# Optimization experiments

Hardware: AMD Instinct MI355X
Metric: run time of the kernel (lower is better)

Reference implementation:

```python
import jax, jax.numpy as jnp
import numpy as np

D_MODEL = 1024
NUM_HEADS = 16
D_HEAD = D_MODEL // NUM_HEADS
B, S = 2, 2048


def setup_inputs() -> dict:
    key = jax.random.key(0)
    ks = jax.random.split(key, 12)
    s = 0.02
    return {
        "query": jax.random.normal(ks[0], (B, S, D_MODEL), jnp.float32),
        "key": jax.random.normal(ks[1], (B, S, D_MODEL), jnp.float32),
        "value": jax.random.normal(ks[2], (B, S, D_MODEL), jnp.float32),
        "mask": jnp.ones((B, 1, 1, S), jnp.float32),
        "W_q": jax.random.normal(ks[3], (D_MODEL, D_MODEL), jnp.float32) * s,
        "b_q": jnp.zeros((D_MODEL,), jnp.float32),
        "W_k": jax.random.normal(ks[4], (D_MODEL, D_MODEL), jnp.float32) * s,
        "b_k": jnp.zeros((D_MODEL,), jnp.float32),
        "W_v": jax.random.normal(ks[5], (D_MODEL, D_MODEL), jnp.float32) * s,
        "b_v": jnp.zeros((D_MODEL,), jnp.float32),
        "W_o": jax.random.normal(ks[6], (D_MODEL, D_MODEL), jnp.float32) * s,
        "b_o": jnp.zeros((D_MODEL,), jnp.float32),
    }


def reference(query, key, value, mask, W_q, b_q, W_k, b_k, W_v, b_v, W_o, b_o):
    # Linear projections (torch nn.Linear: x @ W.T + b; here W stored as [in, out])
    q = query @ W_q + b_q
    k = key @ W_k + b_k
    v = value @ W_v + b_v
    # [B, S, D] -> [B, H, S, Dh]
    def split_heads(x):
        b, s, _ = x.shape
        return x.reshape(b, s, NUM_HEADS, D_HEAD).transpose(0, 2, 1, 3)
    q, k, v = split_heads(q), split_heads(k), split_heads(v)
    # scaled dot-product attention; full [B,H,Sq,Sk] matrix (faithful to source)
    logits = jnp.einsum("bhqd,bhkd->bhqk", q, k) / jnp.sqrt(jnp.float32(D_HEAD))
    logits = logits + (1.0 - mask) * (-1e9)
    attn = jax.nn.softmax(logits, axis=-1)
    # dropout is identity in eval mode
    ctx = jnp.einsum("bhqk,bhkd->bhqd", attn, v)
    ctx = ctx.transpose(0, 2, 1, 3).reshape(ctx.shape[0], -1, D_MODEL)
    out = ctx @ W_o + b_o
    return out, attn
```

## Files before the change

### kernel.cpp

```cpp
#include <hip/hip_runtime.h>
#include <hip/hip_bf16.h>

#define BATCH 2
#define SEQ 2048
#define DM 1024
#define NH 16
#define DH 64
#define MTOT (BATCH*SEQ)

typedef __attribute__((ext_vector_type(8))) short bf16x8;
typedef __attribute__((ext_vector_type(4))) float f32x4;
typedef __attribute__((ext_vector_type(16))) float f32x16;
typedef __attribute__((ext_vector_type(4))) float float4v;
typedef __attribute__((ext_vector_type(8))) unsigned short u16x8;
typedef __attribute__((ext_vector_type(4))) unsigned short u16x4;

#define GLDS16(g, l) __builtin_amdgcn_global_load_lds(                         \
    (const __attribute__((address_space(1))) void*)(g),                        \
    (__attribute__((address_space(3))) void*)(l), 16, 0, 0)

static __device__ __forceinline__ float bf2f(unsigned short u) {
    unsigned int x = ((unsigned int)u) << 16;
    float f; __builtin_memcpy(&f, &x, 4); return f;
}
static __device__ __forceinline__ unsigned short f2bf(float f) {
    unsigned int x; __builtin_memcpy(&x, &f, 4);
    x += 0x7fffu + ((x >> 16) & 1);
    return (unsigned short)(x >> 16);
}
static __device__ __forceinline__ unsigned int cvt_pk_bf16(float a, float b) {
    unsigned int r;
    asm volatile("v_cvt_pk_bf16_f32 %0, %1, %2" : "=v"(r) : "v"(a), "v"(b));
    return r;
}

__global__ __launch_bounds__(256) void prep_kernel(
    const float* __restrict__ q, const float* __restrict__ k, const float* __restrict__ v,
    unsigned short* __restrict__ oq, unsigned short* __restrict__ ok_, unsigned short* __restrict__ ov,
    const float* __restrict__ w0, const float* __restrict__ w1,
    const float* __restrict__ w2, const float* __restrict__ w3,
    unsigned short* __restrict__ t0, unsigned short* __restrict__ t1,
    unsigned short* __restrict__ t2, unsigned short* __restrict__ t3) {
    __shared__ float tile[64][65];
    const int bx = blockIdx.x, t = threadIdx.x;
    if (bx < 6144) {
        const int slab = bx >> 11, bxr = bx & 2047;
        const float* in = slab == 0 ? q : (slab == 1 ? k : v);
        unsigned short* out = slab == 0 ? oq : (slab == 1 ? ok_ : ov);
        size_t i = ((size_t)bxr * 256 + t) * 8;
        float4v a = *(const float4v*)(in + i);
        float4v b = *(const float4v*)(in + i + 4);
        u16x8 r;
        r[0]=f2bf(a[0]); r[1]=f2bf(a[1]); r[2]=f2bf(a[2]); r[3]=f2bf(a[3]);
        r[4]=f2bf(b[0]); r[5]=f2bf(b[1]); r[6]=f2bf(b[2]); r[7]=f2bf(b[3]);
        *(u16x8*)(out + i) = r;
    } else {
        const int i2 = bx - 6144;
        const int z = i2 >> 8, rem = i2 & 255;
        const float* w = z==0 ? w0 : z==1 ? w1 : z==2 ? w2 : w3;
        unsigned short* wt = z==0 ? t0 : z==1 ? t1 : z==2 ? t2 : t3;
        const int k0 = (rem & 15) * 64, n0 = (rem >> 4) * 64;
        const int tr = t >> 4, tc = t & 15;
#pragma unroll
        for (int i = 0; i < 4; ++i) {
            float4v val = *(const float4v*)(w + (size_t)(k0 + tr + 16*i) * DM + n0 + tc*4);
            tile[tr + 16*i][tc*4 + 0] = val[0];
            tile[tr + 16*i][tc*4 + 1] = val[1];
            tile[tr + 16*i][tc*4 + 2] = val[2];
            tile[tr + 16*i][tc*4 + 3] = val[3];
        }
        __syncthreads();
#pragma unroll
        for (int i = 0; i < 4; ++i) {
            u16x4 o;
#pragma unroll
            for (int j = 0; j < 4; ++j) o[j] = f2bf(tile[tc*4 + j][tr + 16*i]);
            *(u16x4*)(wt + (size_t)(n0 + tr + 16*i) * DM + k0 + tc*4) = o;
        }
    }
}

template<int OUTMODE>
static __device__ __forceinline__ void gemm_body(
    const unsigned short* __restrict__ A, const unsigned short* __restrict__ Bt,
    const float* __restrict__ bias, void* __restrict__ Cout,
    unsigned short* a_lds, unsigned short* b_lds) {
    constexpr int BM = 128, BN = 64, BK = 64, NT = DM / BK;
    const int tid = threadIdx.x;
    const int m0 = blockIdx.y * BM, n0 = blockIdx.x * BN;
    const int w = tid >> 6, l = tid & 63;
    const int lr = l & 15, lg = l >> 4;
    const int wm = (w >> 1) * 64, wn = (w & 1) * 32;
    f32x4 acc[4][2] = {};

    auto stage = [&](int buf, int kt) {
        const int k0 = kt * BK;
#pragma unroll
        for (int i = 0; i < 4; ++i) {
            int u = i*256 + tid;
            int row = u >> 3, slot = u & 7;
            int sc = (slot ^ (row & 7)) * 8;
            GLDS16(A + (size_t)(m0 + row)*DM + k0 + sc, a_lds + buf*BM*BK + u*8);
        }
#pragma unroll
        for (int i = 0; i < 2; ++i) {
            int u = i*256 + tid;
            int row = u >> 3, slot = u & 7;
            int sc = (slot ^ (row & 7)) * 8;
            GLDS16(Bt + (size_t)(n0 + row)*DM + k0 + sc, b_lds + buf*BN*BK + u*8);
        }
    };

    stage(0, 0);
    for (int kt = 0; kt < NT; ++kt) {
        __syncthreads();
        if (kt < NT-1) stage((kt+1)&1, kt+1);
        const char* ab = (const char*)(a_lds + (kt&1)*BM*BK);
        const char* bb = (const char*)(b_lds + (kt&1)*BN*BK);
        bf16x8 af[4][2], bfr[2][2];
#pragma unroll
        for (int r = 0; r < 4; ++r)
#pragma unroll
            for (int kc = 0; kc < 2; ++kc) {
                int row = wm + r*16 + lr;
                af[r][kc] = *(const bf16x8*)(ab + row*128 + ((kc*64 + lg*16) ^ ((row&7)<<4)));
            }
#pragma unroll
        for (int c = 0; c < 2; ++c)
#pragma unroll
            for (int kc = 0; kc < 2; ++kc) {
                int row = wn + c*16 + lr;
                bfr[c][kc] = *(const bf16x8*)(bb + row*128 + ((kc*64 + lg*16) ^ ((row&7)<<4)));
            }
#pragma unroll
        for (int r = 0; r < 4; ++r)
#pragma unroll
            for (int c = 0; c < 2; ++c)
#pragma unroll
                for (int kc = 0; kc < 2; ++kc)
                    acc[r][c] = __builtin_amdgcn_mfma_f32_16x16x32_bf16(af[r][kc], bfr[c][kc], acc[r][c], 0, 0, 0);
    }

#pragma unroll
    for (int r = 0; r < 4; ++r)
#pragma unroll
        for (int c = 0; c < 2; ++c) {
            int m = m0 + wm + r*16 + lg*4;
            int n = n0 + wn + c*16 + lr;
            float bb = bias[n];
            if constexpr (OUTMODE == 1) {
                float* o = (float*)Cout;
#pragma unroll
                for (int j = 0; j < 4; ++j) o[(size_t)(m+j)*DM + n] = acc[r][c][j] + bb;
            } else if constexpr (OUTMODE == 0) {
                unsigned short* o = (unsigned short*)Cout;
#pragma unroll
                for (int j = 0; j < 4; ++j) o[(size_t)(m+j)*DM + n] = f2bf(acc[r][c][j] + bb);
            } else {
                unsigned short* o = (unsigned short*)Cout;
                int bb_ = m >> 11, kk = m & (SEQ-1);
                int bh = bb_ * NH + (n >> 6), d = n & 63;
                u16x4 ov;
#pragma unroll
                for (int j = 0; j < 4; ++j) ov[j] = f2bf(acc[r][c][j] + bb);
                *(u16x4*)(o + ((size_t)bh*DH + d)*SEQ + kk) = ov;
            }
        }
}

__global__ __launch_bounds__(256, 3) void gemm_qkv_kernel(
    const unsigned short* __restrict__ A0, const unsigned short* __restrict__ A1, const unsigned short* __restrict__ A2,
    const unsigned short* __restrict__ B0, const unsigned short* __restrict__ B1, const unsigned short* __restrict__ B2,
    const float* __restrict__ c0, const float* __restrict__ c1, const float* __restrict__ c2,
    unsigned short* __restrict__ O0, unsigned short* __restrict__ O1, unsigned short* __restrict__ O2) {
    __shared__ __align__(16) unsigned short smem[2*128*64 + 2*64*64];
    const int z = blockIdx.z;
    const unsigned short* A = z==0 ? A0 : z==1 ? A1 : A2;
    const unsigned short* B = z==0 ? B0 : z==1 ? B1 : B2;
    const float* c = z==0 ? c0 : z==1 ? c1 : c2;
    unsigned short* O = z==0 ? O0 : z==1 ? O1 : O2;
    if (z == 2) gemm_body<2>(A, B, c, O, smem, smem + 2*128*64);
    else        gemm_body<0>(A, B, c, O, smem, smem + 2*128*64);
}

__global__ __launch_bounds__(256, 3) void gemm_out_kernel(
    const unsigned short* __restrict__ A, const unsigned short* __restrict__ Bt,
    const float* __restrict__ bias, float* __restrict__ Cout) {
    __shared__ __align__(16) unsigned short smem[2*128*64 + 2*64*64];
    gemm_body<1>(A, Bt, bias, Cout, smem, smem + 2*128*64);
}

__global__ __launch_bounds__(512, 4) void attn_kernel(
    const unsigned short* __restrict__ qw, const unsigned short* __restrict__ kw,
    const unsigned short* __restrict__ vtg, const float* __restrict__ mask,
    float* __restrict__ attn_out, unsigned short* __restrict__ ctx) {
    constexpr int QB = 128, KB = 64, NT2 = SEQ / KB / 2;
    __shared__ __align__(16) unsigned short smem[4*KB*DH + 4*KB*DH + 4096];
    unsigned short* kbuf = smem;
    unsigned short* vbuf = smem + 4*KB*DH;
    float* madd_f = (float*)(smem + 8*KB*DH);
    const int tid = threadIdx.x, w = tid >> 6, l = tid & 63;
    const int hh = w >> 2, ws = w & 3;
    const int q32 = l & 31, hi = l >> 5;
    const int u0 = (blockIdx.x & 7) * 64 + (blockIdx.x >> 3);
    const int qblk = u0 & 15, bh = u0 >> 4;
    const int b = bh >> 4, h = bh & 15;
    const int q0 = qblk * QB;
    const int q = q0 + ws*32 + q32;
    const int kbase = hh * (SEQ/2);

    {
        int idx = tid * 4;
        float4v m4 = *(const float4v*)(mask + (size_t)b*SEQ + idx);
        float4v md;
#pragma unroll
        for (int r = 0; r < 4; ++r) md[r] = (1.0f - m4[r]) * (-1e9f);
        *(float4v*)(madd_f + idx) = md;
    }

    bf16x8 qf[4];
    {
        const unsigned short* qp = qw + ((size_t)(b*SEQ + q))*DM + h*DH + hi*8;
#pragma unroll
        for (int ks = 0; ks < 4; ++ks) {
            bf16x8 t = *(const bf16x8*)(qp + ks*16);
#pragma unroll
            for (int j = 0; j < 8; ++j) t[j] = (short)f2bf(bf2f((unsigned short)t[j]) * 0.125f);
            qf[ks] = t;
        }
    }

    auto stageK = [&](int buf, int kt) {
#pragma unroll
        for (int hf = 0; hf < 2; ++hf) {
            int row = tid >> 3, slot = tid & 7;
            int sc = (slot ^ (row & 7)) * 8;
            const unsigned short* base = kw + ((size_t)(b*SEQ + hf*(SEQ/2) + kt*KB + row))*DM + h*DH;
            GLDS16(base + sc, kbuf + (buf*2 + hf)*KB*DH + tid*8);
        }
    };
    auto stageV = [&](int buf, int kt) {
#pragma unroll
        for (int hf = 0; hf < 2; ++hf) {
            int row = tid >> 3, slot = tid & 7;
            int sc = (slot ^ (row & 7)) * 8;
            const unsigned short* base = vtg + ((size_t)bh*DH + row)*SEQ + hf*(SEQ/2) + kt*KB;
            GLDS16(base + sc, vbuf + (buf*2 + hf)*KB*DH + tid*8);
        }
    };

    float rs = 0.f;
    stageK(0, 0);
    for (int kt = 0; kt < NT2; ++kt) {
        __syncthreads();
        if (kt < NT2-1) stageK((kt+1)&1, kt+1);
        const char* kb = (const char*)(kbuf + ((kt&1)*2 + hh)*KB*DH);
#pragma unroll
        for (int sub = 0; sub < 2; ++sub) {
            f32x16 s = {};
#pragma unroll
            for (int ks = 0; ks < 4; ++ks) {
                int key = sub*32 + q32;
                bf16x8 kf = *(const bf16x8*)(kb + key*128 + ((ks*32 + hi*16) ^ ((key&7)<<4)));
                s = __builtin_amdgcn_mfma_f32_32x32x16_bf16(kf, qf[ks], s, 0, 0, 0);
            }
#pragma unroll
            for (int rq = 0; rq < 4; ++rq) {
                float4v m4 = *(const float4v*)(madd_f + kbase + kt*KB + sub*32 + rq*8 + hi*4);
#pragma unroll
                for (int r = 0; r < 4; ++r)
                    rs += __expf(s[rq*4 + r] + m4[r]);
            }
        }
    }
    rs += __shfl_xor(rs, 32);
    {
        float* rbuf = (float*)smem;
        __syncthreads();
        rbuf[w*64 + l] = rs;
        __syncthreads();
        rs += rbuf[(w ^ 4)*64 + l];
        __syncthreads();
    }
    const float rinv = 1.0f / rs;

    f32x16 oacc[2] = {};
    float* attn_row = attn_out + ((size_t)bh*SEQ + q)*SEQ + kbase;
    stageK(0, 0); stageV(0, 0);
    for (int kt = 0; kt < NT2; ++kt) {
        __syncthreads();
        if (kt < NT2-1) { stageK((kt+1)&1, kt+1); stageV((kt+1)&1, kt+1); }
        const char* kb = (const char*)(kbuf + ((kt&1)*2 + hh)*KB*DH);
        const char* vb = (const char*)(vbuf + ((kt&1)*2 + hh)*KB*DH);
#pragma unroll
        for (int sub = 0; sub < 2; ++sub) {
            f32x16 s = {};
#pragma unroll
            for (int ks = 0; ks < 4; ++ks) {
                int key = sub*32 + q32;
                bf16x8 kf = *(const bf16x8*)(kb + key*128 + ((ks*32 + hi*16) ^ ((key&7)<<4)));
                s = __builtin_amdgcn_mfma_f32_32x32x16_bf16(kf, qf[ks], s, 0, 0, 0);
            }
#pragma unroll
            for (int half = 0; half < 2; ++half) {
                float4v pv0, pv1;
                {
                    const int rq = half*2;
                    float4v m4 = *(const float4v*)(madd_f + kbase + kt*KB + sub*32 + rq*8 + hi*4);
#pragma unroll
                    for (int r = 0; r < 4; ++r) pv0[r] = __expf(s[rq*4 + r] + m4[r]) * rinv;
                    *(float4v*)(attn_row + kt*KB + sub*32 + rq*8 + hi*4) = pv0;
                }
                {
                    const int rq = half*2 + 1;
                    float4v m4 = *(const float4v*)(madd_f + kbase + kt*KB + sub*32 + rq*8 + hi*4);
#pragma unroll
                    for (int r = 0; r < 4; ++r) pv1[r] = __expf(s[rq*4 + r] + m4[r]) * rinv;
                    *(float4v*)(attn_row + kt*KB + sub*32 + rq*8 + hi*4) = pv1;
                }
                unsigned int w0 = cvt_pk_bf16(pv0[0], pv0[1]);
                unsigned int w1 = cvt_pk_bf16(pv0[2], pv0[3]);
                unsigned int w2 = cvt_pk_bf16(pv1[0], pv1[1]);
                unsigned int w3 = cvt_pk_bf16(pv1[2], pv1[3]);
                asm volatile("v_permlane32_swap_b32 %0, %1" : "+v"(w0), "+v"(w2));
                asm volatile("v_permlane32_swap_b32 %0, %1" : "+v"(w1), "+v"(w3));
                union { unsigned int uu[4]; bf16x8 v; } pa;
                pa.uu[0] = w0; pa.uu[1] = w1; pa.uu[2] = w2; pa.uu[3] = w3;
                const int ks4 = sub*2 + half;
#pragma unroll
                for (int dsub = 0; dsub < 2; ++dsub) {
                    int d = dsub*32 + q32;
                    bf16x8 vf = *(const bf16x8*)(vb + d*128 + ((ks4*32 + hi*16) ^ ((d&7)<<4)));
                    oacc[dsub] = __builtin_amdgcn_mfma_f32_32x32x16_bf16(pa.v, vf, oacc[dsub], 0, 0, 0);
                }
            }
        }
    }

    float* cbuf = (float*)smem;
    __syncthreads();
    if (w >= 4) {
        int base = ((w - 4)*64 + l) * 36;
        *(f32x16*)(cbuf + base) = oacc[0];
        *(f32x16*)(cbuf + base + 16) = oacc[1];
    }
    __syncthreads();
    if (w < 4) {
        int base = (w*64 + l) * 36;
        oacc[0] += *(const f32x16*)(cbuf + base);
        oacc[1] += *(const f32x16*)(cbuf + base + 16);
#pragma unroll
        for (int dsub = 0; dsub < 2; ++dsub) {
            int d = h*DH + dsub*32 + q32;
#pragma unroll
            for (int reg = 0; reg < 16; ++reg) {
                int qr = q0 + ws*32 + (reg&3) + 8*(reg>>2) + 4*hi;
                ctx[(size_t)(b*SEQ + qr)*DM + d] = f2bf(oacc[dsub][reg]);
            }
        }
    }
}

extern "C" void kernel_launch(void* const* d_in, const int* in_sizes, int n_in,
                              void* d_out, int out_size, void* d_ws, size_t ws_size,
                              hipStream_t stream) {
    const float* query = (const float*)d_in[0];
    const float* key_  = (const float*)d_in[1];
    const float* value = (const float*)d_in[2];
    const float* mask  = (const float*)d_in[3];
    const float* W_q = (const float*)d_in[4];
    const float* b_q = (const float*)d_in[5];
    const float* W_k = (const float*)d_in[6];
    const float* b_k = (const float*)d_in[7];
    const float* W_v = (const float*)d_in[8];
    const float* b_v = (const float*)d_in[9];
    const float* W_o = (const float*)d_in[10];
    const float* b_o = (const float*)d_in[11];

    char* ws = (char*)d_ws;
    const size_t SZ = (size_t)MTOT * DM * 2;
    unsigned short* xq  = (unsigned short*)(ws);
    unsigned short* xk  = (unsigned short*)(ws + SZ);
    unsigned short* xv  = (unsigned short*)(ws + 2*SZ);
    unsigned short* wtq = (unsigned short*)(ws + 3*SZ);
    unsigned short* wtk = wtq + (size_t)DM*DM;
    unsigned short* wtv = wtk + (size_t)DM*DM;
    unsigned short* wto = wtv + (size_t)DM*DM;
    unsigned short* qws = (unsigned short*)(ws + 4*SZ);
    unsigned short* kws = (unsigned short*)(ws + 5*SZ);
    unsigned short* vtg = (unsigned short*)(ws + 6*SZ);
    unsigned short* ctx = (unsigned short*)(ws + 7*SZ);
    float* out_f  = (float*)d_out;
    float* attn_f = out_f + (size_t)MTOT * DM;

    prep_kernel<<<dim3(7168), 256, 0, stream>>>(query, key_, value, xq, xk, xv,
                                                W_q, W_k, W_v, W_o, wtq, wtk, wtv, wto);
    gemm_qkv_kernel<<<dim3(16, 32, 3), 256, 0, stream>>>(xq, xk, xv, wtq, wtk, wtv,
                                                         b_q, b_k, b_v, qws, kws, vtg);
    attn_kernel<<<dim3(512), 512, 0, stream>>>(qws, kws, vtg, mask, attn_f, ctx);
    gemm_out_kernel<<<dim3(16, 32), 256, 0, stream>>>(ctx, wto, b_o, out_f);
}
```

Baseline: 286.9 us.

## Split attention into separate denominator and output kernels; use nontemporal attn stores

The two-pass attention kernel is split in two. One kernel computes only the softmax row sums (K only, smaller shared memory, higher occupancy bound) and writes reciprocals to workspace. A second kernel reads those reciprocals, writes the probabilities and computes the context. The large attn-matrix stores become nontemporal to avoid polluting cache. This adds a kernel launch and a small global round trip, but lets the lighter pass run at higher occupancy.

```diff
diff --git a/kernel.cpp b/kernel.cpp
--- a/kernel.cpp
+++ b/kernel.cpp
@@ -190,10 +190,93 @@
     gemm_body<1>(A, Bt, bias, Cout, smem, smem + 2*128*64);
 }
 
-__global__ __launch_bounds__(512, 4) void attn_kernel(
+__global__ __launch_bounds__(512, 6) void attn_den_kernel(
+    const unsigned short* __restrict__ qw, const unsigned short* __restrict__ kw,
+    const float* __restrict__ mask, float* __restrict__ rinv_out) {
+    constexpr int QB = 128, KB = 64, NT2 = SEQ / KB / 2;
+    __shared__ __align__(16) unsigned short smem[4*KB*DH + 4096];
+    unsigned short* kbuf = smem;
+    float* madd_f = (float*)(smem + 4*KB*DH);
+    const int tid = threadIdx.x, w = tid >> 6, l = tid & 63;
+    const int hh = w >> 2, ws = w & 3;
+    const int q32 = l & 31, hi = l >> 5;
+    const int u0 = (blockIdx.x & 7) * 64 + (blockIdx.x >> 3);
+    const int qblk = u0 & 15, bh = u0 >> 4;
+    const int b = bh >> 4, h = bh & 15;
+    const int q0 = qblk * QB;
+    const int q = q0 + ws*32 + q32;
+    const int kbase = hh * (SEQ/2);
+
+    {
+        int idx = tid * 4;
+        float4v m4 = *(const float4v*)(mask + (size_t)b*SEQ + idx);
+        float4v md;
+#pragma unroll
+        for (int r = 0; r < 4; ++r) md[r] = (1.0f - m4[r]) * (-1e9f);
+        *(float4v*)(madd_f + idx) = md;
+    }
+
+    bf16x8 qf[4];
+    {
+        const unsigned short* qp = qw + ((size_t)(b*SEQ + q))*DM + h*DH + hi*8;
+#pragma unroll
+        for (int ks = 0; ks < 4; ++ks) {
+            bf16x8 t = *(const bf16x8*)(qp + ks*16);
+#pragma unroll
+            for (int j = 0; j < 8; ++j) t[j] = (short)f2bf(bf2f((unsigned short)t[j]) * 0.125f);
+            qf[ks] = t;
+        }
+    }
+
+    auto stageK = [&](int buf, int kt) {
+#pragma unroll
+        for (int hf = 0; hf < 2; ++hf) {
+            int row = tid >> 3, slot = tid & 7;
+            int sc = (slot ^ (row & 7)) * 8;
+            const unsigned short* base = kw + ((size_t)(b*SEQ + hf*(SEQ/2) + kt*KB + row))*DM + h*DH;
+            GLDS16(base + sc, kbuf + (buf*2 + hf)*KB*DH + tid*8);
+        }
+    };
+
+    float rs = 0.f;
+    stageK(0, 0);
+    for (int kt = 0; kt < NT2; ++kt) {
+        __syncthreads();
+        if (kt < NT2-1) stageK((kt+1)&1, kt+1);
+        const char* kb = (const char*)(kbuf + ((kt&1)*2 + hh)*KB*DH);
+#pragma unroll
+        for (int sub = 0; sub < 2; ++sub) {
+            f32x16 s = {};
+#pragma unroll
+            for (int ks = 0; ks < 4; ++ks) {
+                int key = sub*32 + q32;
+                bf16x8 kf = *(const bf16x8*)(kb + key*128 + ((ks*32 + hi*16) ^ ((key&7)<<4)));
+                s = __builtin_amdgcn_mfma_f32_32x32x16_bf16(kf, qf[ks], s, 0, 0, 0);
+            }
+#pragma unroll
+            for (int rq = 0; rq < 4; ++rq) {
+                float4v m4 = *(const float4v*)(madd_f + kbase + kt*KB + sub*32 + rq*8 + hi*4);
+#pragma unroll
+                for (int r = 0; r < 4; ++r)
+                    rs += __expf(s[rq*4 + r] + m4[r]);
+            }
+        }
+    }
+    rs += __shfl_xor(rs, 32);
+    float* rbuf = (float*)smem;
+    __syncthreads();
+    rbuf[w*64 + l] = rs;
+    __syncthreads();
+    rs += rbuf[(w ^ 4)*64 + l];
+    if (hh == 0 && l < 32)
+        rinv_out[(size_t)bh*SEQ + q] = 1.0f / rs;
+}
+
+__global__ __launch_bounds__(512, 4) void attn_out_kernel(
     const unsigned short* __restrict__ qw, const unsigned short* __restrict__ kw,
     const unsigned short* __restrict__ vtg, const float* __restrict__ mask,
-    float* __restrict__ attn_out, unsigned short* __restrict__ ctx) {
+    const float* __restrict__ rinv_g, float* __restrict__ attn_out,
+    unsigned short* __restrict__ ctx) {
     constexpr int QB = 128, KB = 64, NT2 = SEQ / KB / 2;
     __shared__ __align__(16) unsigned short smem[4*KB*DH + 4*KB*DH + 4096];
     unsigned short* kbuf = smem;
@@ -217,6 +300,7 @@
         for (int r = 0; r < 4; ++r) md[r] = (1.0f - m4[r]) * (-1e9f);
         *(float4v*)(madd_f + idx) = md;
     }
+    const float rinv = rinv_g[(size_t)bh*SEQ + q];
 
     bf16x8 qf[4];
     {
@@ -248,41 +332,6 @@
             GLDS16(base + sc, vbuf + (buf*2 + hf)*KB*DH + tid*8);
         }
     };
-
-    float rs = 0.f;
-    stageK(0, 0);
-    for (int kt = 0; kt < NT2; ++kt) {
-        __syncthreads();
-        if (kt < NT2-1) stageK((kt+1)&1, kt+1);
-        const char* kb = (const char*)(kbuf + ((kt&1)*2 + hh)*KB*DH);
-#pragma unroll
-        for (int sub = 0; sub < 2; ++sub) {
-            f32x16 s = {};
-#pragma unroll
-            for (int ks = 0; ks < 4; ++ks) {
-                int key = sub*32 + q32;
-                bf16x8 kf = *(const bf16x8*)(kb + key*128 + ((ks*32 + hi*16) ^ ((key&7)<<4)));
-                s = __builtin_amdgcn_mfma_f32_32x32x16_bf16(kf, qf[ks], s, 0, 0, 0);
-            }
-#pragma unroll
-            for (int rq = 0; rq < 4; ++rq) {
-                float4v m4 = *(const float4v*)(madd_f + kbase + kt*KB + sub*32 + rq*8 + hi*4);
-#pragma unroll
-                for (int r = 0; r < 4; ++r)
-                    rs += __expf(s[rq*4 + r] + m4[r]);
-            }
-        }
-    }
-    rs += __shfl_xor(rs, 32);
-    {
-        float* rbuf = (float*)smem;
-        __syncthreads();
-        rbuf[w*64 + l] = rs;
-        __syncthreads();
-        rs += rbuf[(w ^ 4)*64 + l];
-        __syncthreads();
-    }
-    const float rinv = 1.0f / rs;
 
     f32x16 oacc[2] = {};
     float* attn_row = attn_out + ((size_t)bh*SEQ + q)*SEQ + kbase;
@@ -309,14 +358,14 @@
                     float4v m4 = *(const float4v*)(madd_f + kbase + kt*KB + sub*32 + rq*8 + hi*4);
 #pragma unroll
                     for (int r = 0; r < 4; ++r) pv0[r] = __expf(s[rq*4 + r] + m4[r]) * rinv;
-                    *(float4v*)(attn_row + kt*KB + sub*32 + rq*8 + hi*4) = pv0;
+                    __builtin_nontemporal_store(pv0, (float4v*)(attn_row + kt*KB + sub*32 + rq*8 + hi*4));
                 }
                 {
                     const int rq = half*2 + 1;
                     float4v m4 = *(const float4v*)(madd_f + kbase + kt*KB + sub*32 + rq*8 + hi*4);
 #pragma unroll
                     for (int r = 0; r < 4; ++r) pv1[r] = __expf(s[rq*4 + r] + m4[r]) * rinv;
-                    *(float4v*)(attn_row + kt*KB + sub*32 + rq*8 + hi*4) = pv1;
+                    __builtin_nontemporal_store(pv1, (float4v*)(attn_row + kt*KB + sub*32 + rq*8 + hi*4));
                 }
                 unsigned int w0 = cvt_pk_bf16(pv0[0], pv0[1]);
                 unsigned int w1 = cvt_pk_bf16(pv0[2], pv0[3]);
@@ -390,6 +439,7 @@
     unsigned short* kws = (unsigned short*)(ws + 5*SZ);
     unsigned short* vtg = (unsigned short*)(ws + 6*SZ);
     unsigned short* ctx = (unsigned short*)(ws + 7*SZ);
+    float* rinv = (float*)(ws + 8*SZ);
     float* out_f  = (float*)d_out;
     float* attn_f = out_f + (size_t)MTOT * DM;
 
@@ -397,6 +447,7 @@
                                                 W_q, W_k, W_v, W_o, wtq, wtk, wtv, wto);
     gemm_qkv_kernel<<<dim3(16, 32, 3), 256, 0, stream>>>(xq, xk, xv, wtq, wtk, wtv,
                                                          b_q, b_k, b_v, qws, kws, vtg);
-    attn_kernel<<<dim3(512), 512, 0, stream>>>(qws, kws, vtg, mask, attn_f, ctx);
+    attn_den_kernel<<<dim3(512), 512, 0, stream>>>(qws, kws, mask, rinv);
+    attn_out_kernel<<<dim3(512), 512, 0, stream>>>(qws, kws, vtg, mask, rinv, attn_f, ctx);
     gemm_out_kernel<<<dim3(16, 32), 256, 0, stream>>>(ctx, wto, b_o, out_f);
 }
```

Measured after the change: 697.6 us. 143% more time.
